# Kernel optimization log

Measured on AMD Instinct MI355X. Metric: run time of the kernel, lower is better.

The kernel has to match this reference:

```python
import jax, jax.numpy as jnp
import numpy as np
import math

B, T, C = 4, 2048, 768
N_HEAD = 12
HEAD_DIM = C // N_HEAD


def setup_inputs() -> dict:
    key = jax.random.key(0)
    k1, k2, k3, k4, k5 = jax.random.split(key, 5)
    std = 0.02
    x = jax.random.normal(k1, (B, T, C), dtype=jnp.float32)
    W_attn = jax.random.normal(k2, (C, 3 * C), dtype=jnp.float32) * std
    b_attn = jnp.zeros((3 * C,), dtype=jnp.float32)
    W_proj = jax.random.normal(k3, (C, C), dtype=jnp.float32) * std
    b_proj = jnp.zeros((C,), dtype=jnp.float32)
    return {"x": x, "W_attn": W_attn, "b_attn": b_attn,
            "W_proj": W_proj, "b_proj": b_proj}


def reference(x, W_attn, b_attn, W_proj, b_proj):
    b, t, c = x.shape
    h, hd = N_HEAD, c // N_HEAD
    # qkv projection: [B,T,3C] -> q,k,v each [B,H,T,hd]
    qkv = x @ W_attn + b_attn
    qkv = qkv.reshape(b, t, 3, h, hd).transpose(2, 0, 3, 1, 4)  # [3,B,H,T,hd]
    q, k, v = qkv[0], qkv[1], qkv[2]
    scale = 1.0 / math.sqrt(hd)
    # full T x T attention scores (non-flash, as in original)
    attn = jnp.einsum('bhqd,bhkd->bhqk', q, k) * scale  # [B,H,T,T]
    causal = jnp.tril(jnp.ones((t, t), dtype=bool))
    attn = jnp.where(causal[None, None, :, :], attn, -jnp.inf)
    attn = jax.nn.softmax(attn, axis=-1)
    y = jnp.einsum('bhqk,bhkd->bhqd', attn, v)  # [B,H,T,hd]
    y = y.transpose(0, 2, 1, 3).reshape(b, t, c)  # merge heads
    return y @ W_proj + b_proj
```

## Files before the change

kernel.cpp:

```cpp
#include <hip/hip_runtime.h>
#include <hip/hip_bf16.h>
#include <cstdint>

#define B_  4
#define T_  2048
#define C_  768
#define H_  12
#define HD_ 64

#define AS1 __attribute__((address_space(1)))
#define AS3 __attribute__((address_space(3)))

typedef float    f32x4  __attribute__((ext_vector_type(4)));
typedef __bf16   bf16x8 __attribute__((ext_vector_type(8)));
typedef uint32_t u32x4  __attribute__((ext_vector_type(4)));

#define QSCL 0.18033688011112042f
#define MFIX 8.0f

__device__ __forceinline__ uint16_t f2b(float f) {
  __bf16 h = (__bf16)f;
  return __builtin_bit_cast(uint16_t, h);
}
__device__ __forceinline__ uint32_t pk2(float a, float b) {
  return (uint32_t)f2b(a) | ((uint32_t)f2b(b) << 16);
}

__global__ void k_cvt(const float* __restrict__ in, uint16_t* __restrict__ out, int n4) {
  int i = blockIdx.x * blockDim.x + threadIdx.x;
  if (i >= n4) return;
  float4 v = ((const float4*)in)[i];
  uint2 o;
  o.x = pk2(v.x, v.y);
  o.y = pk2(v.z, v.w);
  ((uint2*)out)[i] = o;
}

__global__ void k_tr2(const float* __restrict__ Wa, uint16_t* __restrict__ WtA,
                      const float* __restrict__ Wp, uint16_t* __restrict__ WtP) {
  __shared__ float tile[32][33];
  const int bx = blockIdx.x;
  const float* in;
  uint16_t* out;
  int Cc, n0;
  if (bx < 72) { in = Wa; out = WtA; Cc = 2304; n0 = bx * 32; }
  else         { in = Wp; out = WtP; Cc = 768;  n0 = (bx - 72) * 32; }
  const int k0 = blockIdx.y * 32;
  const int tx = threadIdx.x, ty = threadIdx.y;
#pragma unroll
  for (int i = 0; i < 32; i += 8)
    tile[ty + i][tx] = in[(size_t)(k0 + ty + i) * Cc + n0 + tx];
  __syncthreads();
#pragma unroll
  for (int i = 0; i < 32; i += 8)
    out[(size_t)(n0 + ty + i) * 768 + k0 + tx] = f2b(tile[tx][ty + i]);
}

template <int EPI>
__global__ __launch_bounds__(256, 3) void k_gemm(
    const uint16_t* __restrict__ A, const uint16_t* __restrict__ Bt,
    const float* __restrict__ bias, float* __restrict__ outF,
    uint16_t* __restrict__ outQKV, int M, int N, int K, int nY) {
  __shared__ __align__(16) uint16_t As[3][128 * 32];
  __shared__ __align__(16) uint16_t Bs[3][128 * 32];
  const int nwg = gridDim.x;
  const int bid = blockIdx.x;
  const int wgid = (bid & 7) * (nwg >> 3) + (bid >> 3);
  const int wy = wgid % nY, wx = wgid / nY;

  const int tid  = threadIdx.x;
  const int lane = tid & 63;
  const int wave = tid >> 6;
  const int wrow = (wave >> 1) * 64, wcol = (wave & 1) * 64;
  const int rowBase = wx * 128, colBase = wy * 128;
  const int l16 = lane & 15, kg = lane >> 4;

  f32x4 acc[4][4];
#pragma unroll
  for (int i = 0; i < 4; ++i)
#pragma unroll
    for (int j = 0; j < 4; ++j) acc[i][j] = (f32x4){0.f, 0.f, 0.f, 0.f};

  const int srow  = lane >> 2;
  const int sslot = lane & 3;
  const int ssw   = (sslot ^ (srow & 3)) << 3;

  auto STAGE = [&](int buf, int k0) {
#pragma unroll
    for (int i = 0; i < 2; ++i) {
      const int r = i * 64 + wave * 16 + srow;
      const uint16_t* srcA = A  + (size_t)(rowBase + r) * K + k0 + ssw;
      const uint16_t* srcB = Bt + (size_t)(colBase + r) * K + k0 + ssw;
      uint16_t* dstA = &As[buf][(i * 64 + wave * 16) * 32];
      uint16_t* dstB = &Bs[buf][(i * 64 + wave * 16) * 32];
      __builtin_amdgcn_global_load_lds((const AS1 uint32_t*)srcA, (AS3 uint32_t*)dstA, 16, 0, 0);
      __builtin_amdgcn_global_load_lds((const AS1 uint32_t*)srcB, (AS3 uint32_t*)dstB, 16, 0, 0);
    }
  };

  const int sA = (kg ^ (l16 & 3)) << 3;

  STAGE(0, 0);
  if (32 < K) STAGE(1, 32);
  int t = 0;
  for (int k0 = 0; k0 < K; k0 += 32, ++t) {
    if (k0 + 64 < K) {
      STAGE((t + 2) % 3, k0 + 64);
      asm volatile("s_waitcnt vmcnt(8)" ::: "memory");
    } else if (k0 + 32 < K) {
      asm volatile("s_waitcnt vmcnt(4)" ::: "memory");
    } else {
      asm volatile("s_waitcnt vmcnt(0)" ::: "memory");
    }
    __builtin_amdgcn_sched_barrier(0);
    __builtin_amdgcn_s_barrier();

    const int cb = t % 3;
    bf16x8 af[4], bfv[4];
#pragma unroll
    for (int mi = 0; mi < 4; ++mi)
      af[mi] = *(const bf16x8*)&As[cb][(wrow + mi * 16 + l16) * 32 + sA];
#pragma unroll
    for (int nj = 0; nj < 4; ++nj)
      bfv[nj] = *(const bf16x8*)&Bs[cb][(wcol + nj * 16 + l16) * 32 + sA];
#pragma unroll
    for (int mi = 0; mi < 4; ++mi)
#pragma unroll
      for (int nj = 0; nj < 4; ++nj)
        acc[mi][nj] = __builtin_amdgcn_mfma_f32_16x16x32_bf16(af[mi], bfv[nj], acc[mi][nj], 0, 0, 0);

    __builtin_amdgcn_s_barrier();
  }

  const int rg = lane >> 4;
#pragma unroll
  for (int mi = 0; mi < 4; ++mi)
#pragma unroll
    for (int nj = 0; nj < 4; ++nj) {
      int c = colBase + wcol + nj * 16 + l16;
      float bv = bias[c];
      if (EPI == 0) {
#pragma unroll
        for (int jj = 0; jj < 4; ++jj) {
          int r = rowBase + wrow + mi * 16 + rg * 4 + jj;
          outF[(size_t)r * N + c] = acc[mi][nj][jj] + bv;
        }
      } else {
        int sel = c / 768;
        int rem = c - sel * 768;
        int head = rem >> 6, d = rem & 63;
        int r0 = rowBase + wrow + mi * 16 + rg * 4;
        int bb = r0 >> 11, tt0 = r0 & 2047;
        if (sel == 2) {
          size_t off = (((size_t)2 * (B_ * H_) + bb * H_ + head) * HD_ + d) * T_ + tt0;
          uint2 w;
          w.x = pk2(acc[mi][nj][0] + bv, acc[mi][nj][1] + bv);
          w.y = pk2(acc[mi][nj][2] + bv, acc[mi][nj][3] + bv);
          *(uint2*)&outQKV[off] = w;
        } else {
          float scl = (sel == 0) ? QSCL : 1.0f;
#pragma unroll
          for (int jj = 0; jj < 4; ++jj) {
            size_t off = (((size_t)sel * (B_ * H_) + bb * H_ + head) * T_ + tt0 + jj) * HD_ + d;
            outQKV[off] = f2b((acc[mi][nj][jj] + bv) * scl);
          }
        }
      }
    }
}

__global__ __launch_bounds__(256, 4) void k_attn2(
    const uint16_t* __restrict__ Qb, const uint16_t* __restrict__ Kb,
    const uint16_t* __restrict__ Vb, uint16_t* __restrict__ Y) {
  __shared__ __align__(16) uint16_t Ks[2][64 * 64];
  __shared__ __align__(16) uint16_t Vs[2][64 * 64];
  __shared__ __align__(16) uint16_t Ps[4][16 * 64];
  const int tid  = threadIdx.x;
  const int lane = tid & 63;
  const int wq   = tid >> 6;
  const int l16  = lane & 15, kg = lane >> 4;

  const int idx = blockIdx.x;
  const int tq  = idx >> 3;
  const int px  = tq & 15;
  const int g   = (idx & 7) + 8 * (tq >> 4);
  const int h = g % H_, b = g / H_;
  const size_t headBase = ((size_t)(b * H_ + h)) * (size_t)(T_ * HD_);

  const int srow0 = wq * 16 + (lane >> 3);
  const int sslot = lane & 7;
  const int swz = (l16 & 7) << 2;

  uint32_t* pwords = (uint32_t*)&Ps[wq][0];

  auto STAGE = [&](int buf, int t) {
    const int kvoff = t * 64;
#pragma unroll
    for (int j = 0; j < 2; ++j) {
      const int r  = srow0 + j * 8;
      const int sw = ((sslot ^ (r & 7)) << 3);
      const uint16_t* srcK = Kb + headBase + (size_t)(kvoff + r) * HD_ + sw;
      const uint16_t* srcV = Vb + headBase + (size_t)r * T_ + kvoff + sw;
      uint16_t* dstK = &Ks[buf][(wq * 16 + j * 8) * 64];
      uint16_t* dstV = &Vs[buf][(wq * 16 + j * 8) * 64];
      __builtin_amdgcn_global_load_lds((const AS1 uint32_t*)srcK, (AS3 uint32_t*)dstK, 16, 0, 0);
      __builtin_amdgcn_global_load_lds((const AS1 uint32_t*)srcV, (AS3 uint32_t*)dstV, 16, 0, 0);
    }
  };

  int cur = 0;
  for (int part = 0; part < 2; ++part) {
    const int qb = part ? (31 - px) : px;
    const int qrow0 = qb * 64 + wq * 16;

    bf16x8 qf[2];
    {
      const uint16_t* qp = Qb + headBase + (size_t)(qrow0 + l16) * HD_;
      qf[0] = *(const bf16x8*)(qp + kg * 8);
      qf[1] = *(const bf16x8*)(qp + 32 + kg * 8);
    }

    f32x4 o[4];
#pragma unroll
    for (int i = 0; i < 4; ++i) o[i] = (f32x4){0.f, 0.f, 0.f, 0.f};
    f32x4 lacc = (f32x4){0.f, 0.f, 0.f, 0.f};

    const int nt = qb + 1;
    __syncthreads();
    STAGE(cur, 0);

    for (int t = 0; t < nt; ++t) {
      __syncthreads();
      if (t + 1 < nt) STAGE(cur ^ 1, t + 1);

      const uint16_t* KT = &Ks[cur][0];
      const uint16_t* VT = &Vs[cur][0];

      f32x4 sm[4];
      __builtin_amdgcn_s_setprio(1);
#pragma unroll
      for (int nj = 0; nj < 4; ++nj) {
        f32x4 acc = (f32x4){0.f, 0.f, 0.f, 0.f};
#pragma unroll
        for (int kc = 0; kc < 2; ++kc) {
          const int row = nj * 16 + l16;
          const int s = (((kc * 4 + kg) ^ (row & 7)) << 3);
          bf16x8 kf = *(const bf16x8*)&KT[row * 64 + s];
          acc = __builtin_amdgcn_mfma_f32_16x16x32_bf16(kf, qf[kc], acc, 0, 0, 0);
        }
        sm[nj] = acc;
      }
      __builtin_amdgcn_s_setprio(0);

      if (t == qb) {
        const int kvb = t * 64 + kg * 4;
        const int qg  = qrow0 + l16;
#pragma unroll
        for (int nj = 0; nj < 4; ++nj)
#pragma unroll
          for (int jj = 0; jj < 4; ++jj)
            if (kvb + nj * 16 + jj > qg) sm[nj][jj] = -__builtin_inff();
      }

#pragma unroll
      for (int nj = 0; nj < 4; ++nj) {
#pragma unroll
        for (int jj = 0; jj < 4; ++jj)
          sm[nj][jj] = __builtin_exp2f(sm[nj][jj] - MFIX);
        lacc += sm[nj];
      }

#pragma unroll
      for (int nj = 0; nj < 4; ++nj) {
        uint2 w;
        w.x = pk2(sm[nj][0], sm[nj][1]);
        w.y = pk2(sm[nj][2], sm[nj][3]);
        const int cs = (nj * 8 + kg * 2) ^ swz;
        *(uint2*)&pwords[l16 * 32 + cs] = w;
      }

      __builtin_amdgcn_s_setprio(1);
#pragma unroll
      for (int kc = 0; kc < 2; ++kc) {
        const int cr = (kc * 16 + kg * 4) ^ swz;
        bf16x8 pa = *(const bf16x8*)&pwords[l16 * 32 + cr];
#pragma unroll
        for (int njd = 0; njd < 4; ++njd) {
          const int row = njd * 16 + l16;
          const int s = (((kc * 4 + kg) ^ (row & 7)) << 3);
          bf16x8 vf = *(const bf16x8*)&VT[row * 64 + s];
          o[njd] = __builtin_amdgcn_mfma_f32_16x16x32_bf16(vf, pa, o[njd], 0, 0, 0);
        }
      }
      __builtin_amdgcn_s_setprio(0);

      cur ^= 1;
    }

    float l_ = (lacc[0] + lacc[1]) + (lacc[2] + lacc[3]);
    l_ += __shfl_xor(l_, 16);
    l_ += __shfl_xor(l_, 32);
    float inv = __builtin_amdgcn_rcpf(l_);
    const int q = qrow0 + l16;
    uint16_t* yp = Y + ((size_t)(b * T_ + q)) * C_ + h * HD_ + kg * 4;
#pragma unroll
    for (int njd = 0; njd < 4; ++njd) {
      uint2 w;
      w.x = pk2(o[njd][0] * inv, o[njd][1] * inv);
      w.y = pk2(o[njd][2] * inv, o[njd][3] * inv);
      *(uint2*)(yp + njd * 16) = w;
    }
  }
}

extern "C" void kernel_launch(void* const* d_in, const int* in_sizes, int n_in,
                              void* d_out, int out_size, void* d_ws, size_t ws_size,
                              hipStream_t stream) {
  const float* x      = (const float*)d_in[0];
  const float* W_attn = (const float*)d_in[1];
  const float* b_attn = (const float*)d_in[2];
  const float* W_proj = (const float*)d_in[3];
  const float* b_proj = (const float*)d_in[4];
  float* out = (float*)d_out;

  char* ws = (char*)d_ws;
  uint16_t* xb  = (uint16_t*)(ws);
  uint16_t* WtA = (uint16_t*)(ws + 12582912);
  uint16_t* WtP = (uint16_t*)(ws + 16121856);
  uint16_t* QKV = (uint16_t*)(ws + 17301504);
  uint16_t* Yb  = (uint16_t*)(ws + 55050240);

  uint16_t* Qp = QKV;
  uint16_t* Kp = QKV + 6291456;
  uint16_t* Vp = QKV + 12582912;

  k_cvt<<<6144, 256, 0, stream>>>(x, xb, 1572864);
  k_tr2<<<dim3(96, 24), dim3(32, 8), 0, stream>>>(W_attn, WtA, W_proj, WtP);
  k_gemm<1><<<1152, 256, 0, stream>>>(xb, WtA, b_attn, nullptr, QKV, 8192, 2304, 768, 18);
  k_attn2<<<768, 256, 0, stream>>>(Qp, Kp, Vp, Yb);
  k_gemm<0><<<384, 256, 0, stream>>>(Yb, WtP, b_proj, out, nullptr, 8192, 768, 768, 6);
}
```

Baseline: 139.9 us.

## Split attention KV tile across two wave groups with LDS reduction

Doubles the attention block to 512 threads. Each of the four query-row waves now has a partner wave, and the pair splits the 64-wide KV tile into two 32-column halves, each doing half the QK and PV MFMAs. The partial outputs and row sums of the second half are reduced through LDS, reusing the K/V buffers, before normalisation and store. This adds waves per block to hide latency and shortens the per-wave critical path, at the cost of an extra reduction phase, two more barriers per query block, and duplicated Q loads.

```diff
diff --git a/kernel.cpp b/kernel.cpp
--- a/kernel.cpp
+++ b/kernel.cpp
@@ -169,15 +169,17 @@
     }
 }
 
-__global__ __launch_bounds__(256, 4) void k_attn2(
+__global__ __launch_bounds__(512, 6) void k_attn2(
     const uint16_t* __restrict__ Qb, const uint16_t* __restrict__ Kb,
     const uint16_t* __restrict__ Vb, uint16_t* __restrict__ Y) {
   __shared__ __align__(16) uint16_t Ks[2][64 * 64];
   __shared__ __align__(16) uint16_t Vs[2][64 * 64];
-  __shared__ __align__(16) uint16_t Ps[4][16 * 64];
+  __shared__ __align__(16) uint32_t Pw[8][16 * 20];
   const int tid  = threadIdx.x;
   const int lane = tid & 63;
   const int wq   = tid >> 6;
+  const int qw   = wq & 3;
+  const int kh   = wq >> 2;
   const int l16  = lane & 15, kg = lane >> 4;
 
   const int idx = blockIdx.x;
@@ -187,31 +189,26 @@
   const int h = g % H_, b = g / H_;
   const size_t headBase = ((size_t)(b * H_ + h)) * (size_t)(T_ * HD_);
 
-  const int srow0 = wq * 16 + (lane >> 3);
+  const int srow0 = tid >> 3;
   const int sslot = lane & 7;
-  const int swz = (l16 & 7) << 2;
-
-  uint32_t* pwords = (uint32_t*)&Ps[wq][0];
+  const int ssw   = ((sslot ^ (srow0 & 7)) << 3);
+
+  uint32_t* pw = &Pw[wq][0];
 
   auto STAGE = [&](int buf, int t) {
     const int kvoff = t * 64;
-#pragma unroll
-    for (int j = 0; j < 2; ++j) {
-      const int r  = srow0 + j * 8;
-      const int sw = ((sslot ^ (r & 7)) << 3);
-      const uint16_t* srcK = Kb + headBase + (size_t)(kvoff + r) * HD_ + sw;
-      const uint16_t* srcV = Vb + headBase + (size_t)r * T_ + kvoff + sw;
-      uint16_t* dstK = &Ks[buf][(wq * 16 + j * 8) * 64];
-      uint16_t* dstV = &Vs[buf][(wq * 16 + j * 8) * 64];
-      __builtin_amdgcn_global_load_lds((const AS1 uint32_t*)srcK, (AS3 uint32_t*)dstK, 16, 0, 0);
-      __builtin_amdgcn_global_load_lds((const AS1 uint32_t*)srcV, (AS3 uint32_t*)dstV, 16, 0, 0);
-    }
+    const uint16_t* srcK = Kb + headBase + (size_t)(kvoff + srow0) * HD_ + ssw;
+    const uint16_t* srcV = Vb + headBase + (size_t)srow0 * T_ + kvoff + ssw;
+    uint16_t* dstK = &Ks[buf][(wq * 8) * 64];
+    uint16_t* dstV = &Vs[buf][(wq * 8) * 64];
+    __builtin_amdgcn_global_load_lds((const AS1 uint32_t*)srcK, (AS3 uint32_t*)dstK, 16, 0, 0);
+    __builtin_amdgcn_global_load_lds((const AS1 uint32_t*)srcV, (AS3 uint32_t*)dstV, 16, 0, 0);
   };
 
   int cur = 0;
   for (int part = 0; part < 2; ++part) {
     const int qb = part ? (31 - px) : px;
-    const int qrow0 = qb * 64 + wq * 16;
+    const int qrow0 = qb * 64 + qw * 16;
 
     bf16x8 qf[2];
     {
@@ -236,14 +233,14 @@
       const uint16_t* KT = &Ks[cur][0];
       const uint16_t* VT = &Vs[cur][0];
 
-      f32x4 sm[4];
+      f32x4 sm[2];
       __builtin_amdgcn_s_setprio(1);
 #pragma unroll
-      for (int nj = 0; nj < 4; ++nj) {
+      for (int nj = 0; nj < 2; ++nj) {
         f32x4 acc = (f32x4){0.f, 0.f, 0.f, 0.f};
+        const int row = kh * 32 + nj * 16 + l16;
 #pragma unroll
         for (int kc = 0; kc < 2; ++kc) {
-          const int row = nj * 16 + l16;
           const int s = (((kc * 4 + kg) ^ (row & 7)) << 3);
           bf16x8 kf = *(const bf16x8*)&KT[row * 64 + s];
           acc = __builtin_amdgcn_mfma_f32_16x16x32_bf16(kf, qf[kc], acc, 0, 0, 0);
@@ -253,17 +250,17 @@
       __builtin_amdgcn_s_setprio(0);
 
       if (t == qb) {
-        const int kvb = t * 64 + kg * 4;
+        const int kvb = t * 64 + kh * 32 + kg * 4;
         const int qg  = qrow0 + l16;
 #pragma unroll
-        for (int nj = 0; nj < 4; ++nj)
+        for (int nj = 0; nj < 2; ++nj)
 #pragma unroll
           for (int jj = 0; jj < 4; ++jj)
             if (kvb + nj * 16 + jj > qg) sm[nj][jj] = -__builtin_inff();
       }
 
 #pragma unroll
-      for (int nj = 0; nj < 4; ++nj) {
+      for (int nj = 0; nj < 2; ++nj) {
 #pragma unroll
         for (int jj = 0; jj < 4; ++jj)
           sm[nj][jj] = __builtin_exp2f(sm[nj][jj] - MFIX);
@@ -271,26 +268,21 @@
       }
 
 #pragma unroll
-      for (int nj = 0; nj < 4; ++nj) {
+      for (int nj = 0; nj < 2; ++nj) {
         uint2 w;
         w.x = pk2(sm[nj][0], sm[nj][1]);
         w.y = pk2(sm[nj][2], sm[nj][3]);
-        const int cs = (nj * 8 + kg * 2) ^ swz;
-        *(uint2*)&pwords[l16 * 32 + cs] = w;
+        *(uint2*)&pw[l16 * 20 + nj * 8 + kg * 2] = w;
       }
 
       __builtin_amdgcn_s_setprio(1);
-#pragma unroll
-      for (int kc = 0; kc < 2; ++kc) {
-        const int cr = (kc * 16 + kg * 4) ^ swz;
-        bf16x8 pa = *(const bf16x8*)&pwords[l16 * 32 + cr];
-#pragma unroll
-        for (int njd = 0; njd < 4; ++njd) {
-          const int row = njd * 16 + l16;
-          const int s = (((kc * 4 + kg) ^ (row & 7)) << 3);
-          bf16x8 vf = *(const bf16x8*)&VT[row * 64 + s];
-          o[njd] = __builtin_amdgcn_mfma_f32_16x16x32_bf16(vf, pa, o[njd], 0, 0, 0);
-        }
+      bf16x8 pa = *(const bf16x8*)&pw[l16 * 20 + kg * 4];
+#pragma unroll
+      for (int njd = 0; njd < 4; ++njd) {
+        const int row = njd * 16 + l16;
+        const int s = (((kh * 4 + kg) ^ (row & 7)) << 3);
+        bf16x8 vf = *(const bf16x8*)&VT[row * 64 + s];
+        o[njd] = __builtin_amdgcn_mfma_f32_16x16x32_bf16(vf, pa, o[njd], 0, 0, 0);
       }
       __builtin_amdgcn_s_setprio(0);
 
@@ -300,15 +292,29 @@
     float l_ = (lacc[0] + lacc[1]) + (lacc[2] + lacc[3]);
     l_ += __shfl_xor(l_, 16);
     l_ += __shfl_xor(l_, 32);
-    float inv = __builtin_amdgcn_rcpf(l_);
-    const int q = qrow0 + l16;
-    uint16_t* yp = Y + ((size_t)(b * T_ + q)) * C_ + h * HD_ + kg * 4;
-#pragma unroll
-    for (int njd = 0; njd < 4; ++njd) {
-      uint2 w;
-      w.x = pk2(o[njd][0] * inv, o[njd][1] * inv);
-      w.y = pk2(o[njd][2] * inv, o[njd][3] * inv);
-      *(uint2*)(yp + njd * 16) = w;
+
+    __syncthreads();
+    f32x4* cO = (f32x4*)&Ks[0][0];
+    float*  cL = (float*)&Vs[0][0];
+    if (kh) {
+#pragma unroll
+      for (int njd = 0; njd < 4; ++njd) cO[(njd * 4 + qw) * 64 + lane] = o[njd];
+      if (lane < 16) cL[qw * 64 + lane] = l_;
+    }
+    __syncthreads();
+    if (!kh) {
+      float lsum = l_ + cL[qw * 64 + l16];
+      float inv = __builtin_amdgcn_rcpf(lsum);
+      const int q = qrow0 + l16;
+      uint16_t* yp = Y + ((size_t)(b * T_ + q)) * C_ + h * HD_ + kg * 4;
+#pragma unroll
+      for (int njd = 0; njd < 4; ++njd) {
+        f32x4 oc = o[njd] + cO[(njd * 4 + qw) * 64 + lane];
+        uint2 w;
+        w.x = pk2(oc[0] * inv, oc[1] * inv);
+        w.y = pk2(oc[2] * inv, oc[3] * inv);
+        *(uint2*)(yp + njd * 16) = w;
+      }
     }
   }
 }
@@ -337,6 +343,6 @@
   k_cvt<<<6144, 256, 0, stream>>>(x, xb, 1572864);
   k_tr2<<<dim3(96, 24), dim3(32, 8), 0, stream>>>(W_attn, WtA, W_proj, WtP);
   k_gemm<1><<<1152, 256, 0, stream>>>(xb, WtA, b_attn, nullptr, QKV, 8192, 2304, 768, 18);
-  k_attn2<<<768, 256, 0, stream>>>(Qp, Kp, Vp, Yb);
+  k_attn2<<<768, 512, 0, stream>>>(Qp, Kp, Vp, Yb);
   k_gemm<0><<<384, 256, 0, stream>>>(Yb, WtP, b_proj, out, nullptr, 8192, 768, 768, 6);
 }
```

New measurement: 136.7 us. 2.3% less time.
